# Performance work log

Measured on AMD Instinct MI355X. Metric: run time of the kernel, lower is better.

Reference implementation:

```python
import jax, jax.numpy as jnp
import numpy as np

B, C, H, W = 4, 512, 64, 64
CI = C // 2  # inter_channel


def setup_inputs() -> dict:
    key = jax.random.key(0)
    ks = jax.random.split(key, 5)
    x = jax.random.normal(ks[0], (B, C, H, W), dtype=jnp.float32)
    # 1x1 convs with bias=False == channel-mixing matrices (out_ch, in_ch)
    w_phi = jax.random.normal(ks[1], (CI, C), dtype=jnp.float32) * 0.02
    w_theta = jax.random.normal(ks[2], (CI, C), dtype=jnp.float32) * 0.02
    w_g = jax.random.normal(ks[3], (CI, C), dtype=jnp.float32) * 0.02
    w_mask = jax.random.normal(ks[4], (C, CI), dtype=jnp.float32) * 0.02
    return {"x": x, "w_phi": w_phi, "w_theta": w_theta, "w_g": w_g, "w_mask": w_mask}


def reference(x, w_phi, w_theta, w_g, w_mask):
    b, c, h, w = x.shape
    n = h * w
    ci = w_phi.shape[0]
    xf = x.reshape(b, c, n)  # (b, c, N)
    # 1x1 convs as channel matmuls -> (b, ci, N)
    phi = jnp.einsum('oc,bcn->bon', w_phi, xf)
    theta = jnp.einsum('oc,bcn->bon', w_theta, xf)
    g = jnp.einsum('oc,bcn->bon', w_g, xf)
    # f = theta^T @ phi : (b, N, N), unscaled scores
    f = jnp.einsum('bcn,bcm->bnm', theta, phi)
    a = jax.nn.softmax(f, axis=-1)
    # y = a @ g^T, produced directly in (b, ci, N) layout (fuses the permute)
    y = jnp.einsum('bnm,bcm->bcn', a, g)
    # conv_mask: 1x1 conv back to C channels
    out = jnp.einsum('oc,bcn->bon', w_mask, y)
    return out.reshape(b, c, h, w)
```

## Files before the change

kernel.cpp:

```cpp
#include <hip/hip_runtime.h>


#define BB 4
#define CC 512
#define NN_SP 4096
#define CI 256

typedef _Float16 f16x8 __attribute__((ext_vector_type(8)));
typedef float f32x4 __attribute__((ext_vector_type(4)));

__device__ __forceinline__ void async16(const void* gsrc, void* ldst) {
  __builtin_amdgcn_global_load_lds(
      (const __attribute__((address_space(1))) unsigned int*)gsrc,
      (__attribute__((address_space(3))) unsigned int*)ldst, 16, 0, 0);
}

__global__ __launch_bounds__(256) void convert_w(
    const float* __restrict__ wphi, const float* __restrict__ wtheta,
    const float* __restrict__ wg, const float* __restrict__ wmask,
    _Float16* __restrict__ wpt, _Float16* __restrict__ wgh, _Float16* __restrict__ wmh) {
  int i = blockIdx.x * 256 + threadIdx.x;
  if (i < 512 * 512) {
    int row = i >> 9, k = i & 511;
    float v = (row < 256) ? wphi[row * 512 + k] : wtheta[(row - 256) * 512 + k];
    wpt[i] = (_Float16)v;
  } else if (i < 512 * 512 + 256 * 512) {
    int j = i - 512 * 512;
    wgh[j] = (_Float16)wg[j];
  } else {
    int j = i - 512 * 512 - 256 * 512;
    wmh[j] = (_Float16)wmask[j];
  }
}

__global__ __launch_bounds__(256) void transpose_x(const float* __restrict__ x,
                                                   _Float16* __restrict__ xT) {
  __shared__ float tile[64][65];
  const int n0 = blockIdx.x * 64, c0 = blockIdx.y * 64, b = blockIdx.z;
  const int tx = threadIdx.x & 63, ty = threadIdx.x >> 6;
  const float* xb = x + (long long)b * CC * NN_SP;
#pragma unroll
  for (int i = 0; i < 16; ++i) {
    int row = i * 4 + ty;
    tile[row][tx] = xb[(long long)(c0 + row) * NN_SP + n0 + tx];
  }
  __syncthreads();
  _Float16* xTb = xT + (long long)b * NN_SP * CC;
#pragma unroll
  for (int i = 0; i < 16; ++i) {
    int row = i * 4 + ty;
    xTb[(long long)(n0 + row) * CC + c0 + tx] = (_Float16)tile[tx][row];
  }
}

template <int M, int NT, int K, bool F16OUT>
__global__ __launch_bounds__(256, 2) void gemm_bt(
    const _Float16* __restrict__ Ab, const _Float16* __restrict__ Btb,
    void* __restrict__ Cb, long long sA, long long sB, long long sC) {
  __shared__ _Float16 As[128 * 32];
  __shared__ _Float16 Bs[128 * 32];
  const int tid = threadIdx.x, lane = tid & 63, w = tid >> 6;
  const int wm = w >> 1, wn = w & 1;
  const int l15 = lane & 15, lq = lane >> 4;
  const int b = blockIdx.z;
  const _Float16* A = Ab + (long long)b * sA;
  const _Float16* Bt = Btb + (long long)b * sB;
  const int m0 = blockIdx.y * 128, n0 = blockIdx.x * 128;

  f32x4 acc[4][4];
#pragma unroll
  for (int i = 0; i < 4; ++i)
#pragma unroll
    for (int j = 0; j < 4; ++j) acc[i][j] = (f32x4){0.f, 0.f, 0.f, 0.f};

  for (int k0 = 0; k0 < K; k0 += 32) {
    __syncthreads();
#pragma unroll
    for (int j = 0; j < 2; ++j) {
      int chw = j * 256 + w * 64;
      int ch = chw + lane;
      int row = ch >> 2, kc = ch & 3;
      async16(A + (long long)(m0 + row) * K + k0 + kc * 8, (void*)(As + chw * 8));
      async16(Bt + (long long)(n0 + row) * K + k0 + kc * 8, (void*)(Bs + chw * 8));
    }
    __syncthreads();
    f16x8 af[4], bf[4];
#pragma unroll
    for (int mt = 0; mt < 4; ++mt)
      af[mt] = *(const f16x8*)(As + (wm * 64 + mt * 16 + l15) * 32 + lq * 8);
#pragma unroll
    for (int nt = 0; nt < 4; ++nt)
      bf[nt] = *(const f16x8*)(Bs + (wn * 64 + nt * 16 + l15) * 32 + lq * 8);
#pragma unroll
    for (int mt = 0; mt < 4; ++mt)
#pragma unroll
      for (int nt = 0; nt < 4; ++nt)
        acc[mt][nt] = __builtin_amdgcn_mfma_f32_16x16x32_f16(af[mt], bf[nt], acc[mt][nt], 0, 0, 0);
  }

#pragma unroll
  for (int mt = 0; mt < 4; ++mt)
#pragma unroll
    for (int nt = 0; nt < 4; ++nt)
#pragma unroll
      for (int r = 0; r < 4; ++r) {
        int row = m0 + wm * 64 + mt * 16 + lq * 4 + r;
        int col = n0 + wn * 64 + nt * 16 + l15;
        if (F16OUT)
          ((_Float16*)Cb + (long long)b * sC)[(long long)row * NT + col] = (_Float16)acc[mt][nt][r];
        else
          ((float*)Cb + (long long)b * sC)[(long long)row * NT + col] = acc[mt][nt][r];
      }
}

__global__ __launch_bounds__(512, 2) void flash_attn3(
    const _Float16* __restrict__ pt, const _Float16* __restrict__ g,
    _Float16* __restrict__ yT) {
  __shared__ _Float16 Stg[2][3][8192];
  __shared__ _Float16 Ps[8][2048];
  const int tid = threadIdx.x, lane = tid & 63, w = tid >> 6;
  const int hw = w >> 2, wp = w & 3;
  const int l15 = lane & 15, lq = lane >> 4;

  const int idx = blockIdx.x;
  const int b = (idx >> 1) & 3;
  const int q0 = (((idx >> 3) << 1) | (idx & 1)) * 64;
  const int kvbase = hw * 2048;
  const _Float16* __restrict__ ptb = pt + (long long)b * NN_SP * 512;
  const _Float16* __restrict__ gb = g + (long long)b * CI * NN_SP;

  int offPhi[4], offG[4], chw_[4];
#pragma unroll
  for (int j = 0; j < 4; ++j) {
    int u = wp * 256 + j * 64 + lane;
    chw_[j] = wp * 256 + j * 64;
    int k2 = u >> 9, nv8 = (u >> 6) & 7, r15 = (u >> 2) & 15, rq = u & 3;
    offPhi[j] = (nv8 * 16 + r15) * 512 + k2 * 32 + rq * 8;
    int kq = u >> 8, ct4 = (u >> 6) & 3;
    offG[j] = (ct4 * 16 + r15) * 4096 + kq * 32 + rq * 8;
  }

  f16x8 qreg[8];
#pragma unroll
  for (int kk = 0; kk < 8; ++kk)
    qreg[kk] = *(const f16x8*)(
        ptb + (long long)(q0 + wp * 16 + l15) * 512 + 256 + kk * 32 + lq * 8);

  f32x4 yacc[16];
#pragma unroll
  for (int nt = 0; nt < 16; ++nt) yacc[nt] = (f32x4){0.f, 0.f, 0.f, 0.f};
  float mrow[4] = {-3e38f, -3e38f, -3e38f, -3e38f};
  float lrow[4] = {0.f, 0.f, 0.f, 0.f};

  auto issue = [&](int q, int bi) {
    if (q >= 128) return;
    _Float16* buf = Stg[hw][bi];
    int tq = q >> 3, sub = q & 7, kv0 = kvbase + tq * 128;
    if (sub < 4) {
      const _Float16* basep = ptb + kv0 * 512 + sub * 64;
#pragma unroll
      for (int j = 0; j < 4; ++j)
        async16(basep + offPhi[j], (void*)(buf + chw_[j] * 8));
    } else {
      const _Float16* baseg = gb + (sub - 4) * 64 * 4096 + kv0;
#pragma unroll
      for (int j = 0; j < 4; ++j)
        async16(baseg + offG[j], (void*)(buf + chw_[j] * 8));
    }
  };

  int p = 0, bcur = 0;
  issue(0, 0);
  issue(1, 1);

  for (int t = 0; t < 16; ++t) {
    f32x4 S[8];
#pragma unroll
    for (int i = 0; i < 8; ++i) S[i] = (f32x4){0.f, 0.f, 0.f, 0.f};

#pragma unroll
    for (int c = 0; c < 4; ++c) {
      asm volatile("s_waitcnt vmcnt(4)" ::: "memory");
      asm volatile("s_barrier" ::: "memory");
      int bn = bcur + 2; if (bn >= 3) bn -= 3;
      issue(p + 2, bn);
      const _Float16* buf = Stg[hw][bcur];
#pragma unroll
      for (int k2 = 0; k2 < 2; ++k2)
#pragma unroll
        for (int nv = 0; nv < 8; ++nv) {
          f16x8 bf = *(const f16x8*)(buf + (k2 * 512 + nv * 64 + l15 * 4 + lq) * 8);
          S[nv] = __builtin_amdgcn_mfma_f32_16x16x32_f16(qreg[c * 2 + k2], bf, S[nv], 0, 0, 0);
        }
      ++p; ++bcur; if (bcur == 3) bcur = 0;
    }

    float alpha[4];
#pragma unroll
    for (int r = 0; r < 4; ++r) {
      float mx = fmaxf(fmaxf(S[0][r], S[1][r]), fmaxf(S[2][r], S[3][r]));
      mx = fmaxf(mx, fmaxf(fmaxf(S[4][r], S[5][r]), fmaxf(S[6][r], S[7][r])));
#pragma unroll
      for (int d = 1; d < 16; d <<= 1) mx = fmaxf(mx, __shfl_xor(mx, d, 64));
      float nm = fmaxf(mrow[r], mx);
      alpha[r] = __expf(mrow[r] - nm);
      mrow[r] = nm;
      float ps = 0.f;
#pragma unroll
      for (int nv = 0; nv < 8; ++nv) {
        float pv = __expf(S[nv][r] - nm);
        S[nv][r] = pv;
        ps += pv;
      }
#pragma unroll
      for (int d = 1; d < 16; d <<= 1) ps += __shfl_xor(ps, d, 64);
      lrow[r] = lrow[r] * alpha[r] + ps;
    }
    {
      f32x4 al = {alpha[0], alpha[1], alpha[2], alpha[3]};
#pragma unroll
      for (int nt = 0; nt < 16; ++nt) yacc[nt] *= al;
    }

#pragma unroll
    for (int nv = 0; nv < 8; ++nv) {
      int kq = nv >> 1;
      int lqr = (nv & 1) * 2 + (l15 >> 3);
      int e = l15 & 7;
#pragma unroll
      for (int r = 0; r < 4; ++r) {
        int u = kq * 64 + lqr * 16 + lq * 4 + r;
        Ps[w][u * 8 + e] = (_Float16)S[nv][r];
      }
    }
    f16x8 aP[4];
#pragma unroll
    for (int kq = 0; kq < 4; ++kq)
      aP[kq] = *(const f16x8*)(&Ps[w][(kq * 64 + lane) * 8]);

#pragma unroll
    for (int cg = 0; cg < 4; ++cg) {
      if (t == 15 && cg == 3) {
        asm volatile("s_waitcnt vmcnt(0)" ::: "memory");
      } else {
        asm volatile("s_waitcnt vmcnt(4)" ::: "memory");
      }
      asm volatile("s_barrier" ::: "memory");
      int bn = bcur + 2; if (bn >= 3) bn -= 3;
      issue(p + 2, bn);
      const _Float16* buf = Stg[hw][bcur];
#pragma unroll
      for (int kq = 0; kq < 4; ++kq)
#pragma unroll
        for (int ct = 0; ct < 4; ++ct) {
          f16x8 bf = *(const f16x8*)(buf + (kq * 256 + ct * 64 + l15 * 4 + lq) * 8);
          yacc[cg * 4 + ct] =
              __builtin_amdgcn_mfma_f32_16x16x32_f16(aP[kq], bf, yacc[cg * 4 + ct], 0, 0, 0);
        }
      ++p; ++bcur; if (bcur == 3) bcur = 0;
    }
  }

  __syncthreads();
  float* mbuf = (float*)Stg;
  float* sbuf = (float*)((char*)Stg + 81920);
  if (hw == 1) {
#pragma unroll
    for (int r = 0; r < 4; ++r) {
      int rr = wp * 16 + lq * 4 + r;
#pragma unroll
      for (int nt = 0; nt < 16; ++nt)
        mbuf[rr * 257 + nt * 16 + l15] = yacc[nt][r];
      if (l15 == 0) {
        sbuf[rr * 2 + 0] = mrow[r];
        sbuf[rr * 2 + 1] = lrow[r];
      }
    }
  }
  __syncthreads();
  if (hw == 0) {
    _Float16* yTb = yT + (long long)b * NN_SP * CI;
#pragma unroll
    for (int r = 0; r < 4; ++r) {
      int rr = wp * 16 + lq * 4 + r;
      float m2 = sbuf[rr * 2 + 0], l2 = sbuf[rr * 2 + 1];
      float m = fmaxf(mrow[r], m2);
      float w1 = __expf(mrow[r] - m), w2 = __expf(m2 - m);
      float inv = 1.f / (w1 * lrow[r] + w2 * l2);
      int row = q0 + rr;
#pragma unroll
      for (int nt = 0; nt < 16; ++nt) {
        float v2 = mbuf[rr * 257 + nt * 16 + l15];
        yTb[(long long)row * CI + nt * 16 + l15] =
            (_Float16)((w1 * yacc[nt][r] + w2 * v2) * inv);
      }
    }
  }
}

extern "C" void kernel_launch(void* const* d_in, const int* in_sizes, int n_in,
                              void* d_out, int out_size, void* d_ws, size_t ws_size,
                              hipStream_t stream) {
  const float* x = (const float*)d_in[0];
  const float* w_phi = (const float*)d_in[1];
  const float* w_theta = (const float*)d_in[2];
  const float* w_g = (const float*)d_in[3];
  const float* w_mask = (const float*)d_in[4];
  float* out = (float*)d_out;
  char* ws = (char*)d_ws;

  _Float16* xT = (_Float16*)(ws);
  _Float16* pt = (_Float16*)(ws + 16777216);
  _Float16* gB = (_Float16*)(ws + 33554432);
  _Float16* yT = (_Float16*)(ws + 41943040);
  _Float16* wpt = (_Float16*)(ws + 50331648);
  _Float16* wg = (_Float16*)(ws + 50855936);
  _Float16* wm = (_Float16*)(ws + 51118080);

  convert_w<<<2048, 256, 0, stream>>>(w_phi, w_theta, w_g, w_mask, wpt, wg, wm);
  transpose_x<<<dim3(64, 8, 4), 256, 0, stream>>>(x, xT);
  gemm_bt<4096, 512, 512, true><<<dim3(4, 32, 4), 256, 0, stream>>>(
      xT, wpt, pt, 4096LL * 512, 0, 4096LL * 512);
  gemm_bt<256, 4096, 512, true><<<dim3(32, 2, 4), 256, 0, stream>>>(
      wg, xT, gB, 0, 4096LL * 512, 256LL * 4096);
  flash_attn3<<<dim3(256), 512, 0, stream>>>(pt, gB, yT);
  gemm_bt<512, 4096, 256, false><<<dim3(32, 4, 4), 256, 0, stream>>>(
      wm, yT, out, 0, 4096LL * 256, 512LL * 4096);
}
```

Before: 287.7 us.

## Switch flash attention staging to double-buffered 2-stage chunks with swizzled P buffer

Replaces the triple-buffered pipeline of 8192-element stages with a double buffer of 16384-element stages. Each barrier now covers two sub-tiles, which halves the number of barriers per iteration, and the wait becomes vmcnt(0). It also XOR-swizzles the per-warp P staging in LDS to reduce bank conflicts on the write and read. The trade-off is a shallower prefetch: loads are only one stage ahead and each wait drains fully, so latency hiding may get worse.

Result: faster. 273.4 us (-5.0%).

```diff
diff --git a/kernel.cpp b/kernel.cpp
--- a/kernel.cpp
+++ b/kernel.cpp
@@ -116,7 +116,7 @@
 __global__ __launch_bounds__(512, 2) void flash_attn3(
     const _Float16* __restrict__ pt, const _Float16* __restrict__ g,
     _Float16* __restrict__ yT) {
-  __shared__ _Float16 Stg[2][3][8192];
+  __shared__ _Float16 Stg[2][2][16384];
   __shared__ _Float16 Ps[8][2048];
   const int tid = threadIdx.x, lane = tid & 63, w = tid >> 6;
   const int hw = w >> 2, wp = w & 3;
@@ -152,26 +152,29 @@
   float mrow[4] = {-3e38f, -3e38f, -3e38f, -3e38f};
   float lrow[4] = {0.f, 0.f, 0.f, 0.f};
 
-  auto issue = [&](int q, int bi) {
-    if (q >= 128) return;
-    _Float16* buf = Stg[hw][bi];
-    int tq = q >> 3, sub = q & 7, kv0 = kvbase + tq * 128;
-    if (sub < 4) {
-      const _Float16* basep = ptb + kv0 * 512 + sub * 64;
-#pragma unroll
-      for (int j = 0; j < 4; ++j)
-        async16(basep + offPhi[j], (void*)(buf + chw_[j] * 8));
-    } else {
-      const _Float16* baseg = gb + (sub - 4) * 64 * 4096 + kv0;
-#pragma unroll
-      for (int j = 0; j < 4; ++j)
-        async16(baseg + offG[j], (void*)(buf + chw_[j] * 8));
+  auto issue = [&](int mq, int bi) {
+    if (mq >= 64) return;
+    int t = mq >> 2, mp = mq & 3, kv0 = kvbase + t * 128;
+#pragma unroll
+    for (int hh = 0; hh < 2; ++hh) {
+      int sub = mp * 2 + hh;
+      _Float16* buf = Stg[hw][bi] + hh * 8192;
+      if (sub < 4) {
+        const _Float16* basep = ptb + (long long)kv0 * 512 + sub * 64;
+#pragma unroll
+        for (int j = 0; j < 4; ++j)
+          async16(basep + offPhi[j], (void*)(buf + chw_[j] * 8));
+      } else {
+        const _Float16* baseg = gb + (long long)(sub - 4) * 64 * 4096 + kv0;
+#pragma unroll
+        for (int j = 0; j < 4; ++j)
+          async16(baseg + offG[j], (void*)(buf + chw_[j] * 8));
+      }
     }
   };
 
-  int p = 0, bcur = 0;
+  int p = 0;
   issue(0, 0);
-  issue(1, 1);
 
   for (int t = 0; t < 16; ++t) {
     f32x4 S[8];
@@ -179,20 +182,24 @@
     for (int i = 0; i < 8; ++i) S[i] = (f32x4){0.f, 0.f, 0.f, 0.f};
 
 #pragma unroll
-    for (int c = 0; c < 4; ++c) {
-      asm volatile("s_waitcnt vmcnt(4)" ::: "memory");
+    for (int mp = 0; mp < 2; ++mp) {
+      asm volatile("s_waitcnt vmcnt(0)" ::: "memory");
       asm volatile("s_barrier" ::: "memory");
-      int bn = bcur + 2; if (bn >= 3) bn -= 3;
-      issue(p + 2, bn);
-      const _Float16* buf = Stg[hw][bcur];
-#pragma unroll
-      for (int k2 = 0; k2 < 2; ++k2)
-#pragma unroll
-        for (int nv = 0; nv < 8; ++nv) {
-          f16x8 bf = *(const f16x8*)(buf + (k2 * 512 + nv * 64 + l15 * 4 + lq) * 8);
-          S[nv] = __builtin_amdgcn_mfma_f32_16x16x32_f16(qreg[c * 2 + k2], bf, S[nv], 0, 0, 0);
-        }
-      ++p; ++bcur; if (bcur == 3) bcur = 0;
+      issue(p + 1, (p + 1) & 1);
+      const _Float16* bufb = Stg[hw][p & 1];
+#pragma unroll
+      for (int hh = 0; hh < 2; ++hh) {
+        int c = mp * 2 + hh;
+        const _Float16* buf = bufb + hh * 8192;
+#pragma unroll
+        for (int k2 = 0; k2 < 2; ++k2)
+#pragma unroll
+          for (int nv = 0; nv < 8; ++nv) {
+            f16x8 bf = *(const f16x8*)(buf + (k2 * 512 + nv * 64 + l15 * 4 + lq) * 8);
+            S[nv] = __builtin_amdgcn_mfma_f32_16x16x32_f16(qreg[c * 2 + k2], bf, S[nv], 0, 0, 0);
+          }
+      }
+      ++p;
     }
 
     float alpha[4];
@@ -230,34 +237,38 @@
 #pragma unroll
       for (int r = 0; r < 4; ++r) {
         int u = kq * 64 + lqr * 16 + lq * 4 + r;
-        Ps[w][u * 8 + e] = (_Float16)S[nv][r];
+        int us = u ^ ((u >> 3) & 7);
+        Ps[w][us * 8 + e] = (_Float16)S[nv][r];
       }
     }
     f16x8 aP[4];
 #pragma unroll
-    for (int kq = 0; kq < 4; ++kq)
-      aP[kq] = *(const f16x8*)(&Ps[w][(kq * 64 + lane) * 8]);
-
-#pragma unroll
-    for (int cg = 0; cg < 4; ++cg) {
-      if (t == 15 && cg == 3) {
-        asm volatile("s_waitcnt vmcnt(0)" ::: "memory");
-      } else {
-        asm volatile("s_waitcnt vmcnt(4)" ::: "memory");
-      }
+    for (int kq = 0; kq < 4; ++kq) {
+      int ur = kq * 64 + lane;
+      int urs = ur ^ ((ur >> 3) & 7);
+      aP[kq] = *(const f16x8*)(&Ps[w][urs * 8]);
+    }
+
+#pragma unroll
+    for (int mp = 0; mp < 2; ++mp) {
+      asm volatile("s_waitcnt vmcnt(0)" ::: "memory");
       asm volatile("s_barrier" ::: "memory");
-      int bn = bcur + 2; if (bn >= 3) bn -= 3;
-      issue(p + 2, bn);
-      const _Float16* buf = Stg[hw][bcur];
-#pragma unroll
-      for (int kq = 0; kq < 4; ++kq)
-#pragma unroll
-        for (int ct = 0; ct < 4; ++ct) {
-          f16x8 bf = *(const f16x8*)(buf + (kq * 256 + ct * 64 + l15 * 4 + lq) * 8);
-          yacc[cg * 4 + ct] =
-              __builtin_amdgcn_mfma_f32_16x16x32_f16(aP[kq], bf, yacc[cg * 4 + ct], 0, 0, 0);
-        }
-      ++p; ++bcur; if (bcur == 3) bcur = 0;
+      issue(p + 1, (p + 1) & 1);
+      const _Float16* bufb = Stg[hw][p & 1];
+#pragma unroll
+      for (int hh = 0; hh < 2; ++hh) {
+        int cg = mp * 2 + hh;
+        const _Float16* buf = bufb + hh * 8192;
+#pragma unroll
+        for (int kq = 0; kq < 4; ++kq)
+#pragma unroll
+          for (int ct = 0; ct < 4; ++ct) {
+            f16x8 bf = *(const f16x8*)(buf + (kq * 256 + ct * 64 + l15 * 4 + lq) * 8);
+            yacc[cg * 4 + ct] =
+                __builtin_amdgcn_mfma_f32_16x16x32_f16(aP[kq], bf, yacc[cg * 4 + ct], 0, 0, 0);
+          }
+      }
+      ++p;
     }
   }
 
```
